# Optimization experiments

Measured on AMD Instinct MI355X. Metric: run time of the kernel, lower is better.

The kernel has to match this reference:

```python
import jax, jax.numpy as jnp
import numpy as np

N_NODES = 100000
N_EDGES = 800000
FEAT = 128
HID = 128
NUM_CLASSES = 2
NUM_GRAPHS = 64


def setup_inputs() -> dict:
    key = jax.random.key(0)
    ks = jax.random.split(key, 20)
    s_feat = 1.0 / np.sqrt(FEAT)
    s_hid = 1.0 / np.sqrt(HID)
    s_h2 = 1.0 / np.sqrt(HID // 2)
    inp = {
        "x": jax.random.normal(ks[0], (N_NODES, FEAT), jnp.float32),
        "edge_index": jax.random.randint(ks[1], (2, N_EDGES), 0, N_NODES, jnp.int32),
        "batch": jnp.sort(jax.random.randint(ks[2], (N_NODES,), 0, NUM_GRAPHS, jnp.int32)),
        "fc1_w": jax.random.uniform(ks[3], (FEAT, HID), jnp.float32, -s_feat, s_feat),
        "fc1_b": jax.random.uniform(ks[4], (HID,), jnp.float32, -s_feat, s_feat),
        "conv1_rel_w": jax.random.uniform(ks[5], (HID, HID), jnp.float32, -s_hid, s_hid),
        "conv1_rel_b": jax.random.uniform(ks[6], (HID,), jnp.float32, -s_hid, s_hid),
        "conv1_root_w": jax.random.uniform(ks[7], (HID, HID), jnp.float32, -s_hid, s_hid),
        "fc2_w": jax.random.uniform(ks[8], (HID, HID), jnp.float32, -s_hid, s_hid),
        "fc2_b": jax.random.uniform(ks[9], (HID,), jnp.float32, -s_hid, s_hid),
        "conv2_rel_w": jax.random.uniform(ks[10], (HID, HID), jnp.float32, -s_hid, s_hid),
        "conv2_rel_b": jax.random.uniform(ks[11], (HID,), jnp.float32, -s_hid, s_hid),
        "conv2_root_w": jax.random.uniform(ks[12], (HID, HID), jnp.float32, -s_hid, s_hid),
        "fc3_w": jax.random.uniform(ks[13], (HID, HID), jnp.float32, -s_hid, s_hid),
        "fc3_b": jax.random.uniform(ks[14], (HID,), jnp.float32, -s_hid, s_hid),
        "fc4_w": jax.random.uniform(ks[15], (HID, HID // 2), jnp.float32, -s_hid, s_hid),
        "fc4_b": jax.random.uniform(ks[16], (HID // 2,), jnp.float32, -s_hid, s_hid),
        "fc5_w": jax.random.uniform(ks[17], (HID // 2, NUM_CLASSES), jnp.float32, -s_h2, s_h2),
        "fc5_b": jax.random.uniform(ks[18], (NUM_CLASSES,), jnp.float32, -s_h2, s_h2),
    }
    return inp


def reference(x, edge_index, batch,
              fc1_w, fc1_b, conv1_rel_w, conv1_rel_b, conv1_root_w,
              fc2_w, fc2_b, conv2_rel_w, conv2_rel_b, conv2_root_w,
              fc3_w, fc3_b, fc4_w, fc4_b, fc5_w, fc5_b):
    lrelu = lambda z: jax.nn.leaky_relu(z, 0.01)
    src, dst = edge_index[0], edge_index[1]

    def graph_conv(h, rel_w, rel_b, root_w):
        # PyG GraphConv (aggr='add'): sum_{j in N(i)} x_j @ W_rel + b + x_i @ W_root
        msg = h[src]                                               # [E, H] gather
        agg = jax.ops.segment_sum(msg, dst, num_segments=h.shape[0])  # [N, H] scatter-add
        return agg @ rel_w + rel_b + h @ root_w

    h = lrelu(x @ fc1_w + fc1_b)
    h = lrelu(graph_conv(h, conv1_rel_w, conv1_rel_b, conv1_root_w))
    h = lrelu(h @ fc2_w + fc2_b)
    h = lrelu(graph_conv(h, conv2_rel_w, conv2_rel_b, conv2_root_w))

    # global mean pool over graph ids
    sums = jax.ops.segment_sum(h, batch, num_segments=NUM_GRAPHS)              # [G, H]
    cnts = jax.ops.segment_sum(jnp.ones((h.shape[0], 1), h.dtype), batch,
                               num_segments=NUM_GRAPHS)                        # [G, 1]
    g = sums / jnp.maximum(cnts, 1.0)

    g = lrelu(g @ fc3_w + fc3_b)
    g = lrelu(g @ fc4_w + fc4_b)
    return g @ fc5_w + fc5_b
```

## Files before the change

kernel.cpp:

```cpp
#include <hip/hip_runtime.h>
#include <hip/hip_bf16.h>

#define NN 100000
#define NE 800000
#define PCH 16
#define MAXDEG 40

typedef __attribute__((ext_vector_type(8))) short bf16x8;
typedef __attribute__((ext_vector_type(4))) float f32x4;

__device__ __forceinline__ unsigned short f2b(float f){
  unsigned int u = __float_as_uint(f);
  unsigned int r = (u + 0x7FFFu + ((u>>16)&1u)) >> 16;
  return (unsigned short)r;
}
__device__ __forceinline__ float b2f(unsigned int s){
  return __uint_as_float(s<<16);
}
__device__ __forceinline__ float lrelu(float v){ return v > 0.f ? v : 0.01f*v; }

struct WPtrs { const float* src[6]; unsigned short* dst[6]; };
__global__ void wcvt_kernel(WPtrs p, const int* __restrict__ batch, int* __restrict__ gstart, int N){
  int wi = blockIdx.y;
  if (wi == 6){
    if (blockIdx.x == 0){
      int g = threadIdx.x;
      if (g <= 64){
        int lo = 0, hi = N;
        while (lo < hi){ int mid = (lo+hi)>>1; if (batch[mid] < g) lo = mid+1; else hi = mid; }
        gstart[g] = lo;
      }
    }
    return;
  }
  int idx = blockIdx.x*256 + threadIdx.x;
  p.dst[wi][idx] = f2b(p.src[wi][(idx & 127)*128 + (idx >> 7)]);
}

__global__ __launch_bounds__(256) void fc1_fill_kernel(
    const float* __restrict__ x, const unsigned short* __restrict__ W0t,
    const float* __restrict__ bias, unsigned short* __restrict__ outb, int M,
    const int* __restrict__ ei, int* __restrict__ cnt, int* __restrict__ slot, int E)
{
  __shared__ unsigned short sA[128*72];
  __shared__ unsigned short sW[128*72];
  const int bi = blockIdx.x;
  const int role = bi % 3;
  if (role != 0){
    int fi = (bi/3)*2 + (role-1);
    int base = (fi*256 + threadIdx.x)*2;
    if (base + 2 <= E){
      int2 d2 = *(const int2*)&ei[E + base];
      int2 s2 = *(const int2*)&ei[base];
      int p0 = atomicAdd(&cnt[d2.x], 1);
      int p1 = atomicAdd(&cnt[d2.y], 1);
      if (p0 < MAXDEG) slot[d2.x*MAXDEG + p0] = s2.x;
      if (p1 < MAXDEG) slot[d2.y*MAXDEG + p1] = s2.y;
    }
    return;
  }
  const int tid = threadIdx.x;
  const int w = tid >> 6, l = tid & 63;
  const int row0 = (bi/3) * 128;

  f32x4 acc[2][8];
  #pragma unroll
  for (int r=0;r<2;++r)
    #pragma unroll
    for (int n=0;n<8;++n) acc[r][n] = (f32x4){0.f,0.f,0.f,0.f};

  for (int p=0; p<2; ++p){
    const int koff = p * 64;
    __syncthreads();
    #pragma unroll
    for (int it=0; it<4; ++it){
      int idx = it*256 + tid;
      int r = idx >> 3, c = (idx & 7) * 8;
      int grow = row0 + r;
      bf16x8 v;
      if (grow < M){
        float4 f0 = *(const float4*)(x + grow*128 + koff + c);
        float4 f1 = *(const float4*)(x + grow*128 + koff + c + 4);
        v[0]=(short)f2b(f0.x); v[1]=(short)f2b(f0.y); v[2]=(short)f2b(f0.z); v[3]=(short)f2b(f0.w);
        v[4]=(short)f2b(f1.x); v[5]=(short)f2b(f1.y); v[6]=(short)f2b(f1.z); v[7]=(short)f2b(f1.w);
      } else {
        #pragma unroll
        for (int j=0;j<8;++j) v[j]=0;
      }
      *(bf16x8*)&sA[r*72 + c] = v;
    }
    #pragma unroll
    for (int it=0; it<4; ++it){
      int idx = it*256 + tid;
      int r = idx >> 3, c = (idx & 7) * 8;
      *(bf16x8*)&sW[r*72 + c] = *(const bf16x8*)(W0t + r*128 + koff + c);
    }
    __syncthreads();

    #pragma unroll
    for (int kc=0; kc<2; ++kc){
      const int kb = kc*32 + ((l>>4)<<3);
      bf16x8 a0 = *(const bf16x8*)&sA[(w*32 +      (l&15))*72 + kb];
      bf16x8 a1 = *(const bf16x8*)&sA[(w*32 + 16 + (l&15))*72 + kb];
      #pragma unroll
      for (int nf=0; nf<8; ++nf){
        bf16x8 b = *(const bf16x8*)&sW[(nf*16 + (l&15))*72 + kb];
        acc[0][nf] = __builtin_amdgcn_mfma_f32_16x16x32_bf16(a0, b, acc[0][nf], 0, 0, 0);
        acc[1][nf] = __builtin_amdgcn_mfma_f32_16x16x32_bf16(a1, b, acc[1][nf], 0, 0, 0);
      }
    }
  }

  #pragma unroll
  for (int r=0;r<2;++r){
    int rb = row0 + w*32 + r*16 + ((l>>4)<<2);
    #pragma unroll
    for (int nf=0;nf<8;++nf){
      int col = nf*16 + (l&15);
      float bv = bias[col];
      #pragma unroll
      for (int q=0;q<4;++q){
        int rr = rb + q;
        if (rr < M){
          outb[rr*128 + col] = f2b(lrelu(acc[r][nf][q] + bv));
        }
      }
    }
  }
}

__global__ __launch_bounds__(256) void agg_kernel(
    const unsigned short* __restrict__ h, const int* __restrict__ cnt,
    const int* __restrict__ slot, unsigned short* __restrict__ agg, int N){
  int node = (blockIdx.x*4 + threadIdx.y)*2 + (threadIdx.x >> 5);
  if (node >= N) return;
  int hl = threadIdx.x & 31;
  int deg = min(cnt[node], MAXDEG);
  const int* sl = slot + node*MAXDEG;
  float a0=0.f, a1=0.f, a2=0.f, a3=0.f;
  int j = 0;
  for (; j + 8 <= deg; j += 8){
    int4 ia = *(const int4*)&sl[j];
    int4 ib = *(const int4*)&sl[j+4];
    uint2 v0 = *(const uint2*)&h[ia.x*128 + hl*4];
    uint2 v1 = *(const uint2*)&h[ia.y*128 + hl*4];
    uint2 v2 = *(const uint2*)&h[ia.z*128 + hl*4];
    uint2 v3 = *(const uint2*)&h[ia.w*128 + hl*4];
    uint2 v4 = *(const uint2*)&h[ib.x*128 + hl*4];
    uint2 v5 = *(const uint2*)&h[ib.y*128 + hl*4];
    uint2 v6 = *(const uint2*)&h[ib.z*128 + hl*4];
    uint2 v7 = *(const uint2*)&h[ib.w*128 + hl*4];
    a0 += b2f(v0.x&0xffff)+b2f(v1.x&0xffff)+b2f(v2.x&0xffff)+b2f(v3.x&0xffff)
        + b2f(v4.x&0xffff)+b2f(v5.x&0xffff)+b2f(v6.x&0xffff)+b2f(v7.x&0xffff);
    a1 += b2f(v0.x>>16)+b2f(v1.x>>16)+b2f(v2.x>>16)+b2f(v3.x>>16)
        + b2f(v4.x>>16)+b2f(v5.x>>16)+b2f(v6.x>>16)+b2f(v7.x>>16);
    a2 += b2f(v0.y&0xffff)+b2f(v1.y&0xffff)+b2f(v2.y&0xffff)+b2f(v3.y&0xffff)
        + b2f(v4.y&0xffff)+b2f(v5.y&0xffff)+b2f(v6.y&0xffff)+b2f(v7.y&0xffff);
    a3 += b2f(v0.y>>16)+b2f(v1.y>>16)+b2f(v2.y>>16)+b2f(v3.y>>16)
        + b2f(v4.y>>16)+b2f(v5.y>>16)+b2f(v6.y>>16)+b2f(v7.y>>16);
  }
  for (; j + 4 <= deg; j += 4){
    int4 ia = *(const int4*)&sl[j];
    uint2 v0 = *(const uint2*)&h[ia.x*128 + hl*4];
    uint2 v1 = *(const uint2*)&h[ia.y*128 + hl*4];
    uint2 v2 = *(const uint2*)&h[ia.z*128 + hl*4];
    uint2 v3 = *(const uint2*)&h[ia.w*128 + hl*4];
    a0 += b2f(v0.x&0xffff)+b2f(v1.x&0xffff)+b2f(v2.x&0xffff)+b2f(v3.x&0xffff);
    a1 += b2f(v0.x>>16)+b2f(v1.x>>16)+b2f(v2.x>>16)+b2f(v3.x>>16);
    a2 += b2f(v0.y&0xffff)+b2f(v1.y&0xffff)+b2f(v2.y&0xffff)+b2f(v3.y&0xffff);
    a3 += b2f(v0.y>>16)+b2f(v1.y>>16)+b2f(v2.y>>16)+b2f(v3.y>>16);
  }
  for (; j < deg; ++j){
    int s = sl[j];
    uint2 v = *(const uint2*)&h[s*128 + hl*4];
    a0 += b2f(v.x&0xffff); a1 += b2f(v.x>>16);
    a2 += b2f(v.y&0xffff); a3 += b2f(v.y>>16);
  }
  uint2 o;
  o.x = ((unsigned int)f2b(a1) << 16) | f2b(a0);
  o.y = ((unsigned int)f2b(a3) << 16) | f2b(a2);
  *(uint2*)&agg[node*128 + hl*4] = o;
}

__global__ __launch_bounds__(256) void convfc_kernel(
    const unsigned short* __restrict__ A0, const unsigned short* __restrict__ A1,
    const unsigned short* __restrict__ W0t, const unsigned short* __restrict__ W1t,
    const float* __restrict__ bias1,
    const unsigned short* __restrict__ W2t, const float* __restrict__ bias2,
    unsigned short* __restrict__ outb, int M)
{
  __shared__ unsigned short sA[128*72];
  __shared__ unsigned short sW[128*72];
  const int tid = threadIdx.x;
  const int w = tid >> 6, l = tid & 63;
  const int row0 = blockIdx.x * 128;

  bf16x8 pa[4][4];
  #pragma unroll
  for (int p=0; p<4; ++p){
    const unsigned short* Ag = (p>>1) ? A1 : A0;
    const int koff = (p&1)*64;
    #pragma unroll
    for (int it=0; it<4; ++it){
      int idx = it*256 + tid;
      int r = idx >> 3, c = (idx & 7) * 8;
      int grow = row0 + r;
      if (grow < M){
        pa[p][it] = *(const bf16x8*)(Ag + grow*128 + koff + c);
      } else {
        #pragma unroll
        for (int j=0;j<8;++j) pa[p][it][j] = 0;
      }
    }
  }

  f32x4 acc[2][8];
  #pragma unroll
  for (int r=0;r<2;++r)
    #pragma unroll
    for (int n=0;n<8;++n) acc[r][n] = (f32x4){0.f,0.f,0.f,0.f};

  #pragma unroll
  for (int p=0; p<4; ++p){
    const unsigned short* Wt = (p>>1) ? W1t : W0t;
    const int koff = (p&1)*64;
    __syncthreads();
    #pragma unroll
    for (int it=0; it<4; ++it){
      int idx = it*256 + tid;
      int r = idx >> 3, c = (idx & 7) * 8;
      *(bf16x8*)&sA[r*72 + c] = pa[p][it];
      *(bf16x8*)&sW[r*72 + c] = *(const bf16x8*)(Wt + r*128 + koff + c);
    }
    __syncthreads();
    #pragma unroll
    for (int kc=0; kc<2; ++kc){
      const int kb = kc*32 + ((l>>4)<<3);
      bf16x8 a0 = *(const bf16x8*)&sA[(w*32 +      (l&15))*72 + kb];
      bf16x8 a1 = *(const bf16x8*)&sA[(w*32 + 16 + (l&15))*72 + kb];
      #pragma unroll
      for (int nf=0; nf<8; ++nf){
        bf16x8 b = *(const bf16x8*)&sW[(nf*16 + (l&15))*72 + kb];
        acc[0][nf] = __builtin_amdgcn_mfma_f32_16x16x32_bf16(a0, b, acc[0][nf], 0, 0, 0);
        acc[1][nf] = __builtin_amdgcn_mfma_f32_16x16x32_bf16(a1, b, acc[1][nf], 0, 0, 0);
      }
    }
  }

  unsigned short v16[2][8][4];
  #pragma unroll
  for (int r=0;r<2;++r)
    #pragma unroll
    for (int nf=0;nf<8;++nf){
      float bv = bias1[nf*16 + (l&15)];
      #pragma unroll
      for (int q=0;q<4;++q) v16[r][nf][q] = f2b(lrelu(acc[r][nf][q] + bv));
    }

  f32x4 acc2[2][8];
  #pragma unroll
  for (int r=0;r<2;++r)
    #pragma unroll
    for (int n=0;n<8;++n) acc2[r][n] = (f32x4){0.f,0.f,0.f,0.f};

  #pragma unroll
  for (int ph=0; ph<2; ++ph){
    __syncthreads();
    #pragma unroll
    for (int r=0;r<2;++r)
      #pragma unroll
      for (int nfl=0;nfl<4;++nfl){
        int nf = ph*4 + nfl;
        int cl = nfl*16 + (l&15);
        #pragma unroll
        for (int q=0;q<4;++q){
          int row = w*32 + r*16 + ((l>>4)<<2) + q;
          sA[row*72 + cl] = v16[r][nf][q];
        }
      }
    #pragma unroll
    for (int it=0; it<4; ++it){
      int idx = it*256 + tid;
      int r = idx >> 3, c = (idx & 7) * 8;
      *(bf16x8*)&sW[r*72 + c] = *(const bf16x8*)(W2t + r*128 + ph*64 + c);
    }
    __syncthreads();
    #pragma unroll
    for (int kc=0; kc<2; ++kc){
      const int kb = kc*32 + ((l>>4)<<3);
      bf16x8 a0 = *(const bf16x8*)&sA[(w*32 +      (l&15))*72 + kb];
      bf16x8 a1 = *(const bf16x8*)&sA[(w*32 + 16 + (l&15))*72 + kb];
      #pragma unroll
      for (int nf=0; nf<8; ++nf){
        bf16x8 b = *(const bf16x8*)&sW[(nf*16 + (l&15))*72 + kb];
        acc2[0][nf] = __builtin_amdgcn_mfma_f32_16x16x32_bf16(a0, b, acc2[0][nf], 0, 0, 0);
        acc2[1][nf] = __builtin_amdgcn_mfma_f32_16x16x32_bf16(a1, b, acc2[1][nf], 0, 0, 0);
      }
    }
  }

  #pragma unroll
  for (int r=0;r<2;++r){
    int rb = row0 + w*32 + r*16 + ((l>>4)<<2);
    #pragma unroll
    for (int nf=0;nf<8;++nf){
      int col = nf*16 + (l&15);
      float bv = bias2[col];
      #pragma unroll
      for (int q=0;q<4;++q){
        int rr = rb + q;
        if (rr < M){
          outb[rr*128 + col] = f2b(lrelu(acc2[r][nf][q] + bv));
        }
      }
    }
  }
}

__global__ __launch_bounds__(256) void gemm2_kernel(
    const unsigned short* __restrict__ A0, const unsigned short* __restrict__ A1,
    const unsigned short* __restrict__ W0t, const unsigned short* __restrict__ W1t,
    const float* __restrict__ bias, unsigned short* __restrict__ outb, int M)
{
  __shared__ unsigned short sA[128*72];
  __shared__ unsigned short sW[128*72];
  const int tid = threadIdx.x;
  const int w = tid >> 6, l = tid & 63;
  const int row0 = blockIdx.x * 128;

  bf16x8 pa[4][4];
  #pragma unroll
  for (int p=0; p<4; ++p){
    const unsigned short* Ag = (p>>1) ? A1 : A0;
    const int koff = (p&1)*64;
    #pragma unroll
    for (int it=0; it<4; ++it){
      int idx = it*256 + tid;
      int r = idx >> 3, c = (idx & 7) * 8;
      int grow = row0 + r;
      if (grow < M){
        pa[p][it] = *(const bf16x8*)(Ag + grow*128 + koff + c);
      } else {
        #pragma unroll
        for (int j=0;j<8;++j) pa[p][it][j] = 0;
      }
    }
  }

  f32x4 acc[2][8];
  #pragma unroll
  for (int r=0;r<2;++r)
    #pragma unroll
    for (int n=0;n<8;++n) acc[r][n] = (f32x4){0.f,0.f,0.f,0.f};

  #pragma unroll
  for (int p=0; p<4; ++p){
    const unsigned short* Wt = (p>>1) ? W1t : W0t;
    const int koff = (p&1)*64;

    __syncthreads();
    #pragma unroll
    for (int it=0; it<4; ++it){
      int idx = it*256 + tid;
      int r = idx >> 3, c = (idx & 7) * 8;
      *(bf16x8*)&sA[r*72 + c] = pa[p][it];
      *(bf16x8*)&sW[r*72 + c] = *(const bf16x8*)(Wt + r*128 + koff + c);
    }
    __syncthreads();

    #pragma unroll
    for (int kc=0; kc<2; ++kc){
      const int kb = kc*32 + ((l>>4)<<3);
      bf16x8 a0 = *(const bf16x8*)&sA[(w*32 +      (l&15))*72 + kb];
      bf16x8 a1 = *(const bf16x8*)&sA[(w*32 + 16 + (l&15))*72 + kb];
      #pragma unroll
      for (int nf=0; nf<8; ++nf){
        bf16x8 b = *(const bf16x8*)&sW[(nf*16 + (l&15))*72 + kb];
        acc[0][nf] = __builtin_amdgcn_mfma_f32_16x16x32_bf16(a0, b, acc[0][nf], 0, 0, 0);
        acc[1][nf] = __builtin_amdgcn_mfma_f32_16x16x32_bf16(a1, b, acc[1][nf], 0, 0, 0);
      }
    }
  }

  #pragma unroll
  for (int r=0;r<2;++r){
    int rb = row0 + w*32 + r*16 + ((l>>4)<<2);
    #pragma unroll
    for (int nf=0;nf<8;++nf){
      int col = nf*16 + (l&15);
      float bv = bias[col];
      #pragma unroll
      for (int q=0;q<4;++q){
        int rr = rb + q;
        if (rr < M){
          outb[rr*128 + col] = f2b(lrelu(acc[r][nf][q] + bv));
        }
      }
    }
  }
}

__global__ __launch_bounds__(256) void pool_kernel(
    const unsigned short* __restrict__ h, const int* __restrict__ gstart,
    float* __restrict__ gsum){
  int g = blockIdx.y;
  int s = gstart[g], e = gstart[g+1];
  int cnt = e - s;
  if (cnt <= 0) return;
  int len = (cnt + PCH - 1) / PCH;
  int r0 = s + blockIdx.x * len;
  int r1 = min(r0 + len, e);
  int w = threadIdx.x >> 6, l = threadIdx.x & 63;
  float ax = 0.f, ay = 0.f;
  for (int n = r0 + w; n < r1; n += 4){
    unsigned int v = *(const unsigned int*)&h[n*128 + l*2];
    ax += b2f(v & 0xffff);
    ay += b2f(v >> 16);
  }
  __shared__ float sm[4][128];
  sm[w][l*2]   = ax;
  sm[w][l*2+1] = ay;
  __syncthreads();
  int t = threadIdx.x;
  if (t < 128){
    float v = sm[0][t] + sm[1][t] + sm[2][t] + sm[3][t];
    atomicAdd(&gsum[g*128 + t], v);
  }
}

__global__ void head3_kernel(const float* gsum, const int* gstart, const float* w, const float* b, float* g3){
  int g = blockIdx.x, c = threadIdx.x;
  int cnt = gstart[g+1] - gstart[g];
  float inv = 1.f / (float)max(cnt, 1);
  float s = b[c];
  for (int k=0;k<128;++k) s += gsum[g*128+k]*inv * w[k*128 + c];
  g3[g*128 + c] = lrelu(s);
}
__global__ void head4_kernel(const float* g3, const float* w, const float* b, float* g4){
  int g = blockIdx.x, c = threadIdx.x;
  float s = b[c];
  for (int k=0;k<128;++k) s += g3[g*128+k] * w[k*64 + c];
  g4[g*64 + c] = lrelu(s);
}
__global__ void head5_kernel(const float* g4, const float* w, const float* b, float* out){
  int o = threadIdx.x;
  if (o < 128){
    int g = o >> 1, c = o & 1;
    float s = b[c];
    for (int k=0;k<64;++k) s += g4[g*64+k] * w[k*2 + c];
    out[o] = s;
  }
}

extern "C" void kernel_launch(void* const* d_in, const int* in_sizes, int n_in,
                              void* d_out, int out_size, void* d_ws, size_t ws_size,
                              hipStream_t stream){
  const float* x        = (const float*)d_in[0];
  const int*   ei       = (const int*)d_in[1];
  const int*   batch    = (const int*)d_in[2];
  const float* fc1_w    = (const float*)d_in[3];
  const float* fc1_b    = (const float*)d_in[4];
  const float* c1_rel_w = (const float*)d_in[5];
  const float* c1_rel_b = (const float*)d_in[6];
  const float* c1_root_w= (const float*)d_in[7];
  const float* fc2_w    = (const float*)d_in[8];
  const float* fc2_b    = (const float*)d_in[9];
  const float* c2_rel_w = (const float*)d_in[10];
  const float* c2_rel_b = (const float*)d_in[11];
  const float* c2_root_w= (const float*)d_in[12];
  const float* fc3_w    = (const float*)d_in[13];
  const float* fc3_b    = (const float*)d_in[14];
  const float* fc4_w    = (const float*)d_in[15];
  const float* fc4_b    = (const float*)d_in[16];
  const float* fc5_w    = (const float*)d_in[17];
  const float* fc5_b    = (const float*)d_in[18];

  char* ws = (char*)d_ws;
  size_t off = 0;
  auto alloc = [&](size_t bytes)->void*{
    void* p = ws + off;
    off = (off + bytes + 255) & ~(size_t)255;
    return p;
  };
  float* gsum   = (float*)alloc(64*128*4);
  int*   cnt    = (int*)  alloc((size_t)NN*4);
  size_t zero_bytes = off;
  int*   gstart = (int*)  alloc(65*4);
  int*   slot   = (int*)  alloc((size_t)NN*MAXDEG*4);
  unsigned short* Wt[6];
  for (int i=0;i<6;++i) Wt[i] = (unsigned short*)alloc(128*128*2);
  unsigned short* B1 = (unsigned short*)alloc((size_t)NN*128*2);
  unsigned short* B2 = (unsigned short*)alloc((size_t)NN*128*2);
  unsigned short* B3 = (unsigned short*)alloc((size_t)NN*128*2);
  float* g3 = (float*)alloc(64*128*4);
  float* g4 = (float*)alloc(64*64*4);
  (void)ws_size; (void)in_sizes; (void)n_in; (void)out_size;

  hipMemsetAsync(d_ws, 0, zero_bytes, stream);

  WPtrs wp;
  wp.src[0]=fc1_w;    wp.dst[0]=Wt[0];
  wp.src[1]=c1_rel_w; wp.dst[1]=Wt[1];
  wp.src[2]=c1_root_w;wp.dst[2]=Wt[2];
  wp.src[3]=fc2_w;    wp.dst[3]=Wt[3];
  wp.src[4]=c2_rel_w; wp.dst[4]=Wt[4];
  wp.src[5]=c2_root_w;wp.dst[5]=Wt[5];
  wcvt_kernel<<<dim3(64,7), 256, 0, stream>>>(wp, batch, gstart, NN);

  const int GB   = (NN + 127)/128;
  const int AB   = (NN + 7)/8;
  const int FATB = 3*GB;

  fc1_fill_kernel<<<FATB, 256, 0, stream>>>(x, Wt[0], fc1_b, B1, NN, ei, cnt, slot, NE);
  agg_kernel<<<AB, dim3(64,4), 0, stream>>>(B1, cnt, slot, B3, NN);
  convfc_kernel<<<GB, 256, 0, stream>>>(B3, B1, Wt[1], Wt[2], c1_rel_b, Wt[3], fc2_b, B2, NN);
  agg_kernel<<<AB, dim3(64,4), 0, stream>>>(B2, cnt, slot, B3, NN);
  gemm2_kernel<<<GB, 256, 0, stream>>>(B3, B2, Wt[4], Wt[5], c2_rel_b, B1, NN);
  pool_kernel<<<dim3(PCH, 64), 256, 0, stream>>>(B1, gstart, gsum);
  head3_kernel<<<64, 128, 0, stream>>>(gsum, gstart, fc3_w, fc3_b, g3);
  head4_kernel<<<64, 64, 0, stream>>>(g3, fc4_w, fc4_b, g4);
  head5_kernel<<<1, 128, 0, stream>>>(g4, fc5_w, fc5_b, (float*)d_out);
}
```

Baseline: 244.6 us.

## Load GEMM operands directly from global into MFMA fragments, drop LDS staging

The convfc and gemm2 kernels no longer stage the A and W tiles through shared memory. Each lane now loads its MFMA fragments straight from global memory, relying on L1/L2 to serve the weight reuse, with row indices clamped to M-1 instead of zero-padded. This removes the barriers and LDS traffic and cuts LDS usage, which may raise occupancy. In exchange, weight fragments are re-fetched from cache by every wave, and the A loads are less coalesced.

```diff
diff --git a/kernel.cpp b/kernel.cpp
--- a/kernel.cpp
+++ b/kernel.cpp
@@ -190,57 +190,34 @@
     unsigned short* __restrict__ outb, int M)
 {
   __shared__ unsigned short sA[128*72];
-  __shared__ unsigned short sW[128*72];
   const int tid = threadIdx.x;
   const int w = tid >> 6, l = tid & 63;
   const int row0 = blockIdx.x * 128;
-
-  bf16x8 pa[4][4];
+  const int lr  = l & 15;
+  const int kb0 = (l >> 4) * 8;
+
+  const int ra = min(row0 + w*32 +      lr, M-1);
+  const int rb_ = min(row0 + w*32 + 16 + lr, M-1);
+
+  f32x4 acc[2][8];
+  #pragma unroll
+  for (int r=0;r<2;++r)
+    #pragma unroll
+    for (int n=0;n<8;++n) acc[r][n] = (f32x4){0.f,0.f,0.f,0.f};
+
   #pragma unroll
   for (int p=0; p<4; ++p){
     const unsigned short* Ag = (p>>1) ? A1 : A0;
-    const int koff = (p&1)*64;
-    #pragma unroll
-    for (int it=0; it<4; ++it){
-      int idx = it*256 + tid;
-      int r = idx >> 3, c = (idx & 7) * 8;
-      int grow = row0 + r;
-      if (grow < M){
-        pa[p][it] = *(const bf16x8*)(Ag + grow*128 + koff + c);
-      } else {
-        #pragma unroll
-        for (int j=0;j<8;++j) pa[p][it][j] = 0;
-      }
-    }
-  }
-
-  f32x4 acc[2][8];
-  #pragma unroll
-  for (int r=0;r<2;++r)
-    #pragma unroll
-    for (int n=0;n<8;++n) acc[r][n] = (f32x4){0.f,0.f,0.f,0.f};
-
-  #pragma unroll
-  for (int p=0; p<4; ++p){
     const unsigned short* Wt = (p>>1) ? W1t : W0t;
     const int koff = (p&1)*64;
-    __syncthreads();
-    #pragma unroll
-    for (int it=0; it<4; ++it){
-      int idx = it*256 + tid;
-      int r = idx >> 3, c = (idx & 7) * 8;
-      *(bf16x8*)&sA[r*72 + c] = pa[p][it];
-      *(bf16x8*)&sW[r*72 + c] = *(const bf16x8*)(Wt + r*128 + koff + c);
-    }
-    __syncthreads();
     #pragma unroll
     for (int kc=0; kc<2; ++kc){
-      const int kb = kc*32 + ((l>>4)<<3);
-      bf16x8 a0 = *(const bf16x8*)&sA[(w*32 +      (l&15))*72 + kb];
-      bf16x8 a1 = *(const bf16x8*)&sA[(w*32 + 16 + (l&15))*72 + kb];
+      const int kk = koff + kc*32 + kb0;
+      bf16x8 a0 = *(const bf16x8*)(Ag + ra *128 + kk);
+      bf16x8 a1 = *(const bf16x8*)(Ag + rb_*128 + kk);
       #pragma unroll
       for (int nf=0; nf<8; ++nf){
-        bf16x8 b = *(const bf16x8*)&sW[(nf*16 + (l&15))*72 + kb];
+        bf16x8 b = *(const bf16x8*)(Wt + (nf*16 + lr)*128 + kk);
         acc[0][nf] = __builtin_amdgcn_mfma_f32_16x16x32_bf16(a0, b, acc[0][nf], 0, 0, 0);
         acc[1][nf] = __builtin_amdgcn_mfma_f32_16x16x32_bf16(a1, b, acc[1][nf], 0, 0, 0);
       }
@@ -252,7 +229,7 @@
   for (int r=0;r<2;++r)
     #pragma unroll
     for (int nf=0;nf<8;++nf){
-      float bv = bias1[nf*16 + (l&15)];
+      float bv = bias1[nf*16 + lr];
       #pragma unroll
       for (int q=0;q<4;++q) v16[r][nf][q] = f2b(lrelu(acc[r][nf][q] + bv));
     }
@@ -271,28 +248,22 @@
       #pragma unroll
       for (int nfl=0;nfl<4;++nfl){
         int nf = ph*4 + nfl;
-        int cl = nfl*16 + (l&15);
+        int cl = nfl*16 + lr;
         #pragma unroll
         for (int q=0;q<4;++q){
           int row = w*32 + r*16 + ((l>>4)<<2) + q;
           sA[row*72 + cl] = v16[r][nf][q];
         }
       }
-    #pragma unroll
-    for (int it=0; it<4; ++it){
-      int idx = it*256 + tid;
-      int r = idx >> 3, c = (idx & 7) * 8;
-      *(bf16x8*)&sW[r*72 + c] = *(const bf16x8*)(W2t + r*128 + ph*64 + c);
-    }
     __syncthreads();
     #pragma unroll
     for (int kc=0; kc<2; ++kc){
-      const int kb = kc*32 + ((l>>4)<<3);
-      bf16x8 a0 = *(const bf16x8*)&sA[(w*32 +      (l&15))*72 + kb];
-      bf16x8 a1 = *(const bf16x8*)&sA[(w*32 + 16 + (l&15))*72 + kb];
+      const int kb = kc*32 + kb0;
+      bf16x8 a0 = *(const bf16x8*)&sA[(w*32 +      lr)*72 + kb];
+      bf16x8 a1 = *(const bf16x8*)&sA[(w*32 + 16 + lr)*72 + kb];
       #pragma unroll
       for (int nf=0; nf<8; ++nf){
-        bf16x8 b = *(const bf16x8*)&sW[(nf*16 + (l&15))*72 + kb];
+        bf16x8 b = *(const bf16x8*)(W2t + (nf*16 + lr)*128 + ph*64 + kb);
         acc2[0][nf] = __builtin_amdgcn_mfma_f32_16x16x32_bf16(a0, b, acc2[0][nf], 0, 0, 0);
         acc2[1][nf] = __builtin_amdgcn_mfma_f32_16x16x32_bf16(a1, b, acc2[1][nf], 0, 0, 0);
       }
@@ -304,7 +275,7 @@
     int rb = row0 + w*32 + r*16 + ((l>>4)<<2);
     #pragma unroll
     for (int nf=0;nf<8;++nf){
-      int col = nf*16 + (l&15);
+      int col = nf*16 + lr;
       float bv = bias2[col];
       #pragma unroll
       for (int q=0;q<4;++q){
@@ -322,60 +293,34 @@
     const unsigned short* __restrict__ W0t, const unsigned short* __restrict__ W1t,
     const float* __restrict__ bias, unsigned short* __restrict__ outb, int M)
 {
-  __shared__ unsigned short sA[128*72];
-  __shared__ unsigned short sW[128*72];
   const int tid = threadIdx.x;
   const int w = tid >> 6, l = tid & 63;
   const int row0 = blockIdx.x * 128;
-
-  bf16x8 pa[4][4];
+  const int lr  = l & 15;
+  const int kb0 = (l >> 4) * 8;
+
+  const int ra = min(row0 + w*32 +      lr, M-1);
+  const int rb_ = min(row0 + w*32 + 16 + lr, M-1);
+
+  f32x4 acc[2][8];
+  #pragma unroll
+  for (int r=0;r<2;++r)
+    #pragma unroll
+    for (int n=0;n<8;++n) acc[r][n] = (f32x4){0.f,0.f,0.f,0.f};
+
   #pragma unroll
   for (int p=0; p<4; ++p){
     const unsigned short* Ag = (p>>1) ? A1 : A0;
-    const int koff = (p&1)*64;
-    #pragma unroll
-    for (int it=0; it<4; ++it){
-      int idx = it*256 + tid;
-      int r = idx >> 3, c = (idx & 7) * 8;
-      int grow = row0 + r;
-      if (grow < M){
-        pa[p][it] = *(const bf16x8*)(Ag + grow*128 + koff + c);
-      } else {
-        #pragma unroll
-        for (int j=0;j<8;++j) pa[p][it][j] = 0;
-      }
-    }
-  }
-
-  f32x4 acc[2][8];
-  #pragma unroll
-  for (int r=0;r<2;++r)
-    #pragma unroll
-    for (int n=0;n<8;++n) acc[r][n] = (f32x4){0.f,0.f,0.f,0.f};
-
-  #pragma unroll
-  for (int p=0; p<4; ++p){
     const unsigned short* Wt = (p>>1) ? W1t : W0t;
     const int koff = (p&1)*64;
-
-    __syncthreads();
-    #pragma unroll
-    for (int it=0; it<4; ++it){
-      int idx = it*256 + tid;
-      int r = idx >> 3, c = (idx & 7) * 8;
-      *(bf16x8*)&sA[r*72 + c] = pa[p][it];
-      *(bf16x8*)&sW[r*72 + c] = *(const bf16x8*)(Wt + r*128 + koff + c);
-    }
-    __syncthreads();
-
     #pragma unroll
     for (int kc=0; kc<2; ++kc){
-      const int kb = kc*32 + ((l>>4)<<3);
-      bf16x8 a0 = *(const bf16x8*)&sA[(w*32 +      (l&15))*72 + kb];
-      bf16x8 a1 = *(const bf16x8*)&sA[(w*32 + 16 + (l&15))*72 + kb];
+      const int kk = koff + kc*32 + kb0;
+      bf16x8 a0 = *(const bf16x8*)(Ag + ra *128 + kk);
+      bf16x8 a1 = *(const bf16x8*)(Ag + rb_*128 + kk);
       #pragma unroll
       for (int nf=0; nf<8; ++nf){
-        bf16x8 b = *(const bf16x8*)&sW[(nf*16 + (l&15))*72 + kb];
+        bf16x8 b = *(const bf16x8*)(Wt + (nf*16 + lr)*128 + kk);
         acc[0][nf] = __builtin_amdgcn_mfma_f32_16x16x32_bf16(a0, b, acc[0][nf], 0, 0, 0);
         acc[1][nf] = __builtin_amdgcn_mfma_f32_16x16x32_bf16(a1, b, acc[1][nf], 0, 0, 0);
       }
@@ -387,7 +332,7 @@
     int rb = row0 + w*32 + r*16 + ((l>>4)<<2);
     #pragma unroll
     for (int nf=0;nf<8;++nf){
-      int col = nf*16 + (l&15);
+      int col = nf*16 + lr;
       float bv = bias[col];
       #pragma unroll
       for (int q=0;q<4;++q){
```

After: 294.3 us. 20.3% more time.
